# Kernel tuning notes

Hardware: AMD Instinct MI355X
Metric: run time of the kernel (lower is better)

## Reference

```python
import jax, jax.numpy as jnp
import numpy as np

HEADS = 4
C_HEAD = 32


def setup_inputs() -> dict:
    key = jax.random.key(0)
    k1, k2, k3 = jax.random.split(key, 3)
    c_in = 256
    c_hid = HEADS * C_HEAD  # 128
    x = jax.random.normal(k1, (4, c_in, 64, 64), dtype=jnp.float32)
    # 1x1 conv weights stored as [out, in]
    w_qkv = jax.random.normal(k2, (3 * c_hid, c_in), dtype=jnp.float32) * (c_in ** -0.5)
    w_out = jax.random.normal(k3, (c_in, c_hid), dtype=jnp.float32) * (c_hid ** -0.5)
    b_out = jnp.zeros((c_in,), dtype=jnp.float32)
    return {"x": x, "w_qkv": w_qkv, "w_out": w_out, "b_out": b_out}


def reference(x, w_qkv, w_out, b_out):
    b, c, h, w = x.shape
    scale = C_HEAD ** -0.5
    # 1x1 conv == channel matmul
    qkv = jnp.einsum('bchw,oc->bohw', x, w_qkv)  # [b, 3*c_hid, h, w]
    q, k, v = jnp.split(qkv, 3, axis=1)
    # b (heads c_head) x y -> b heads c_head (x y)
    def to_heads(t):
        return t.reshape(b, HEADS, C_HEAD, h * w)
    q, k, v = to_heads(q) * scale, to_heads(k), to_heads(v)
    sim = jnp.einsum('bhci,bhcj->bhij', q, k)  # [b, heads, N, N]
    sim = sim - jax.lax.stop_gradient(jnp.max(sim, axis=-1, keepdims=True))
    attn = jax.nn.softmax(sim, axis=-1)
    out = jnp.einsum('bhij,bhcj->bhic', attn, v)  # [b, heads, N, c_head]
    # b h (x y) c -> b (h c) x y
    out = out.transpose(0, 1, 3, 2).reshape(b, HEADS * C_HEAD, h, w)
    out = jnp.einsum('bchw,oc->bohw', out, w_out) + b_out[None, :, None, None]
    return out
```

## Files before the change

kernel.cpp:

```cpp
#include <hip/hip_runtime.h>
#include <hip/hip_bf16.h>
#include <cstdint>
#include <cstddef>


#define NB 4
#define CIN 256
#define CHID 128
#define HEADS 4
#define CHEAD 32
#define NPOS 4096
#define BH 16
#define NTOT 16384
#define QKV_O 384
#define QSCALE_LOG2E 0.2550348229f

typedef float f32x2 __attribute__((ext_vector_type(2)));
typedef float f32x4 __attribute__((ext_vector_type(4)));
typedef float f32x16 __attribute__((ext_vector_type(16)));
typedef short s16x8 __attribute__((ext_vector_type(8)));

static __device__ __forceinline__ unsigned short f2bf(float f) {
    union { float f; unsigned u; } v; v.f = f;
    unsigned r = v.u + 0x7FFFu + ((v.u >> 16) & 1u);
    return (unsigned short)(r >> 16);
}

static __device__ __forceinline__ unsigned int pk2bf(float a, float b) {
    union { __hip_bfloat162 h; unsigned int u; } c;
    c.h = __float22bfloat162_rn(float2{a, b});
    return c.u;
}

static __device__ __forceinline__ void plswap(unsigned& a, unsigned& b) {
#if __has_builtin(__builtin_amdgcn_permlane32_swap)
    auto r = __builtin_amdgcn_permlane32_swap((int)a, (int)b, false, false);
    a = (unsigned)r[0];
    b = (unsigned)r[1];
#else
    int hh = (threadIdx.x >> 5) & 1;
    unsigned ta = (unsigned)__shfl_xor((int)a, 32);
    unsigned tb = (unsigned)__shfl_xor((int)b, 32);
    unsigned na = hh ? tb : a;
    unsigned nb = hh ? b : ta;
    a = na; b = nb;
#endif
}

static __device__ __forceinline__ s16x8 mk8(unsigned a, unsigned b, unsigned c, unsigned d) {
    union { unsigned u[4]; s16x8 v; } x;
    x.u[0] = a; x.u[1] = b; x.u[2] = c; x.u[3] = d;
    return x.v;
}

static __device__ __forceinline__ void async_cp16(const void* g, void* l) {
    __builtin_amdgcn_global_load_lds((const __attribute__((address_space(1))) unsigned int*)g,
                                     (__attribute__((address_space(3))) unsigned int*)l, 16, 0, 0);
}

#define MFMA32(a, b, c) __builtin_amdgcn_mfma_f32_32x32x16_bf16(a, b, c, 0, 0, 0)


#define TBLOCKS (NB * (CIN / 32) * (NPOS / 32))
__global__ __launch_bounds__(256) void k_prep(const float* __restrict__ x,
                                              unsigned short* __restrict__ xT,
                                              const float* __restrict__ wqkv,
                                              const float* __restrict__ wout,
                                              unsigned short* __restrict__ wqkv_bf,
                                              unsigned short* __restrict__ wout_bf) {
    if (blockIdx.x >= TBLOCKS) {
        int i = (blockIdx.x - TBLOCKS) * 256 + threadIdx.x;
        if (i < QKV_O * CIN) wqkv_bf[i] = f2bf(wqkv[i]);
        if (i < CIN * CHID)  wout_bf[i] = f2bf(wout[i]);
        return;
    }
    __shared__ float tile[32][33];
    const int ntiles = NPOS / 32;
    const int ctiles = CIN / 32;
    int b   = blockIdx.x / (ntiles * ctiles);
    int rem = blockIdx.x % (ntiles * ctiles);
    int ct = rem / ntiles;
    int nt = rem % ntiles;
    int c0 = ct * 32, n0 = nt * 32;
    int tc = threadIdx.x / 32;
    int tn = threadIdx.x % 32;
    const float* xb = x + (size_t)b * CIN * NPOS;
#pragma unroll
    for (int it = 0; it < 4; ++it) {
        int c = tc + it * 8;
        tile[c][tn] = xb[(size_t)(c0 + c) * NPOS + n0 + tn];
    }
    __syncthreads();
    unsigned short* xTb = xT + (size_t)b * NPOS * CIN;
#pragma unroll
    for (int it = 0; it < 4; ++it) {
        int n = tc + it * 8;
        xTb[(size_t)(n0 + n) * CIN + c0 + tn] = f2bf(tile[tn][n]);
    }
}

__global__ __launch_bounds__(256, 4) void k_qkv(const unsigned short* __restrict__ wq,
                                                const unsigned short* __restrict__ xT,
                                                unsigned short* __restrict__ Q,
                                                unsigned short* __restrict__ K,
                                                unsigned short* __restrict__ V) {
    __shared__ __align__(16) unsigned char smem[2 * 12288];
    int mt = blockIdx.x % 3;
    int nt = blockIdx.x / 3;
    int wid = threadIdx.x >> 6, lane = threadIdx.x & 63;
    int quad = lane >> 4, low4 = lane & 15;
    int o0 = mt * 128, n0 = nt * 64;
    int lb = lane * 16;

    const unsigned short* srcA0 = wq + (size_t)(o0 + wid * 32 + low4) * CIN + quad * 8;
    const unsigned short* srcA1 = srcA0 + 16 * CIN;
    const unsigned short* srcB  = xT + (size_t)(n0 + wid * 16 + low4) * CIN + quad * 8;
    int dA0 = wid * 2048, dA1 = dA0 + 1024, dB = 8192 + wid * 1024;

    async_cp16(srcA0, smem + dA0 + lb);
    async_cp16(srcA1, smem + dA1 + lb);
    async_cp16(srcB,  smem + dB  + lb);
    __syncthreads();

    f32x4 acc[2][4] = {};
    for (int c = 0; c < 8; ++c) {
        if (c < 7) {
            unsigned char* nxt = smem + ((c + 1) & 1) * 12288;
            async_cp16(srcA0 + (c + 1) * 32, nxt + dA0 + lb);
            async_cp16(srcA1 + (c + 1) * 32, nxt + dA1 + lb);
            async_cp16(srcB  + (c + 1) * 32, nxt + dB  + lb);
        }
        const unsigned char* cur = smem + (c & 1) * 12288;
        s16x8 a0 = *(const s16x8*)(cur + wid * 2048 + lb);
        s16x8 a1 = *(const s16x8*)(cur + wid * 2048 + 1024 + lb);
#pragma unroll
        for (int j = 0; j < 4; ++j) {
            s16x8 bj = *(const s16x8*)(cur + 8192 + j * 1024 + lb);
            acc[0][j] = __builtin_amdgcn_mfma_f32_16x16x32_bf16(a0, bj, acc[0][j], 0, 0, 0);
            acc[1][j] = __builtin_amdgcn_mfma_f32_16x16x32_bf16(a1, bj, acc[1][j], 0, 0, 0);
        }
        __syncthreads();
    }

    if (mt == 0) {
#pragma unroll
        for (int i = 0; i < 2; ++i) {
            int ol = wid * 32 + i * 16 + quad * 4;
            int head = ol >> 5, ch = ol & 31;
#pragma unroll
            for (int j = 0; j < 4; ++j) {
                int nG = n0 + j * 16 + low4;
                int b = nG >> 12, n = nG & 4095;
                f32x4 v = acc[i][j];
                unsigned long long d =
                    (unsigned long long)pk2bf(v[0] * QSCALE_LOG2E, v[1] * QSCALE_LOG2E) |
                    ((unsigned long long)pk2bf(v[2] * QSCALE_LOG2E, v[3] * QSCALE_LOG2E) << 32);
                *(unsigned long long*)(Q + ((size_t)(b * 4 + head) * NPOS + n) * 32 + ch) = d;
            }
        }
    } else if (mt == 1) {
#pragma unroll
        for (int i = 0; i < 2; ++i) {
            int ol = wid * 32 + i * 16 + quad * 4;
            int head = ol >> 5, c0 = ol & 31;
            int f = c0 >> 4, hh = (c0 >> 3) & 1, j8 = c0 & 7;
#pragma unroll
            for (int j = 0; j < 4; ++j) {
                int nG = n0 + j * 16 + low4;
                int b = nG >> 12, n = nG & 4095;
                int bh = b * 4 + head;
                f32x4 v = acc[i][j];
                unsigned long long d =
                    (unsigned long long)pk2bf(v[0], v[1]) |
                    ((unsigned long long)pk2bf(v[2], v[3]) << 32);
                size_t addr = (((size_t)bh * 128 + (n >> 5)) * 2 + f) * 512
                            + (size_t)((((hh << 5) | (n & 31)) << 3) + j8);
                *(unsigned long long*)(K + addr) = d;
            }
        }
    } else {
        unsigned short* vt = (unsigned short*)smem;
#pragma unroll
        for (int i = 0; i < 2; ++i) {
            int ol = wid * 32 + i * 16 + quad * 4;
#pragma unroll
            for (int j = 0; j < 4; ++j) {
                int col = j * 16 + low4;
#pragma unroll
                for (int r = 0; r < 4; ++r) vt[(ol + r) * 80 + col] = f2bf(acc[i][j][r]);
            }
        }
        __syncthreads();
        int b = n0 >> 12, nbase = n0 & 4095;
#pragma unroll
        for (int rep = 0; rep < 4; ++rep) {
            int idx = rep * 256 + threadIdx.x;
            int row = idx >> 3, c8 = idx & 7;
            s16x8 val = *(const s16x8*)(vt + row * 80 + c8 * 8);
            int head = row >> 5, ch = row & 31;
            int bh = b * 4 + head;
            int nstart = nbase + c8 * 8;
            int kc = nstart >> 4, hh = (nstart >> 3) & 1;
            *(s16x8*)(V + ((size_t)(bh * 256 + kc) * 64 + ((hh << 5) | ch)) * 8) = val;
        }
    }
}

__global__ __launch_bounds__(256, 4) void k_attn(const unsigned short* __restrict__ Q,
                                                 const unsigned short* __restrict__ K,
                                                 const unsigned short* __restrict__ V,
                                                 unsigned short* __restrict__ attnO) {
    __shared__ __align__(16) unsigned char smem[2 * 16384];
    int bh = blockIdx.x & 15;
    int qt = blockIdx.x >> 4;
    int wid = threadIdx.x >> 6;
    int lane = threadIdx.x & 63;
    int q5 = lane & 31, h = lane >> 5;
    int qg = wid & 1, kh = wid >> 1;
    int q0 = qt * 64 + qg * 32;
    int khk = kh * 2048;

    const unsigned short* Qp = Q + (size_t)bh * NPOS * 32;

    s16x8 bq0 = *(const s16x8*)(Qp + (size_t)(q0 + q5) * 32 + h * 8);
    s16x8 bq1 = *(const s16x8*)(Qp + (size_t)(q0 + q5) * 32 + 16 + h * 8);

    const unsigned short* pKf = K + (size_t)bh * 131072 + lane * 8;
    const unsigned short* pVf = V + (size_t)bh * 131072 + lane * 8;

    auto stage = [&](int bufi, int k0) {
        unsigned char* wb = smem + bufi * 16384 + kh * 8192;
        if (qg == 0) {
            const unsigned short* p = pKf + (size_t)(k0 >> 5) * 1024;
            async_cp16(p,        wb);
            async_cp16(p + 512,  wb + 1024);
            async_cp16(p + 1024, wb + 2048);
            async_cp16(p + 1536, wb + 3072);
        } else {
            const unsigned short* p = pVf + (size_t)(k0 >> 4) * 512;
            async_cp16(p,        wb + 4096);
            async_cp16(p + 512,  wb + 5120);
            async_cp16(p + 1024, wb + 6144);
            async_cp16(p + 1536, wb + 7168);
        }
    };

    f32x16 oT = {};
    f32x2 lacc0 = {0.0f, 0.0f}, lacc1 = {0.0f, 0.0f};
    const int lby = lane * 16;

    stage(0, khk);

#pragma unroll 1
    for (int it = 0; it < 32; ++it) {
        if (it + 1 < 32) {
            stage((it + 1) & 1, khk + (it + 1) * 64);
            asm volatile("s_waitcnt vmcnt(4)" ::: "memory");
        } else {
            asm volatile("s_waitcnt vmcnt(0)" ::: "memory");
        }
        asm volatile("s_barrier" ::: "memory");

        const unsigned char* kb = smem + (it & 1) * 16384 + kh * 8192;
#pragma unroll
        for (int t = 0; t < 2; ++t) {
            s16x8 ak0 = *(const s16x8*)(kb + t * 2048 + lby);
            s16x8 ak1 = *(const s16x8*)(kb + t * 2048 + 1024 + lby);
            f32x16 s = {};
            __builtin_amdgcn_s_setprio(1);
            s = MFMA32(ak0, bq0, s);
            s = MFMA32(ak1, bq1, s);
            __builtin_amdgcn_s_setprio(0);
            unsigned p[8];
#pragma unroll
            for (int i = 0; i < 8; ++i) {
                float e0 = __builtin_amdgcn_exp2f(s[2 * i]);
                float e1 = __builtin_amdgcn_exp2f(s[2 * i + 1]);
                f32x2 e = {e0, e1};
                if (i & 1) lacc0 += e;
                else       lacc1 += e;
                p[i] = pk2bf(e0, e1);
            }
            plswap(p[0], p[2]); plswap(p[1], p[3]);
            plswap(p[4], p[6]); plswap(p[5], p[7]);
            s16x8 bplo = mk8(p[0], p[1], p[2], p[3]);
            s16x8 bphi = mk8(p[4], p[5], p[6], p[7]);

            s16x8 av0 = *(const s16x8*)(kb + 4096 + (2 * t) * 1024 + lby);
            s16x8 av1 = *(const s16x8*)(kb + 4096 + (2 * t + 1) * 1024 + lby);
            __builtin_amdgcn_s_setprio(1);
            oT = MFMA32(av0, bplo, oT);
            oT = MFMA32(av1, bphi, oT);
            __builtin_amdgcn_s_setprio(0);
        }
        asm volatile("s_barrier" ::: "memory");
    }

    float lsum = lacc0[0] + lacc0[1] + lacc1[0] + lacc1[1];
    lsum += __shfl_xor(lsum, 32);

    if (kh) {
        float* area = (float*)(smem + qg * 4352);
#pragma unroll
        for (int j = 0; j < 4; ++j)
            *(f32x4*)(area + j * 256 + lane * 4) =
                f32x4{oT[4 * j], oT[4 * j + 1], oT[4 * j + 2], oT[4 * j + 3]};
        area[1024 + lane] = lsum;
    }
    __syncthreads();
    if (!kh) {
        const float* area = (const float*)(smem + qg * 4352);
        lsum += area[1024 + lane];
        float inv = 1.0f / lsum;
        int b = bh >> 2, head = bh & 3;
        int n = q0 + q5;
        unsigned short* base = attnO + ((size_t)(b * NPOS + n)) * CHID + head * 32 + 4 * h;
#pragma unroll
        for (int j = 0; j < 4; ++j) {
            f32x4 r = *(const f32x4*)(area + j * 256 + lane * 4);
            unsigned long long d =
                (unsigned long long)pk2bf((oT[4 * j] + r[0]) * inv, (oT[4 * j + 1] + r[1]) * inv) |
                ((unsigned long long)pk2bf((oT[4 * j + 2] + r[2]) * inv, (oT[4 * j + 3] + r[3]) * inv) << 32);
            *(unsigned long long*)(base + 8 * j) = d;
        }
    }
}

__global__ __launch_bounds__(256, 4) void k_out(const unsigned short* __restrict__ wo,
                                                const unsigned short* __restrict__ attnO,
                                                const float* __restrict__ bias,
                                                float* __restrict__ out) {
    __shared__ __align__(16) unsigned char smem[2 * 12288];
    int mt = blockIdx.x & 1;
    int nt = blockIdx.x >> 1;
    int wid = threadIdx.x >> 6, lane = threadIdx.x & 63;
    int quad = lane >> 4, low4 = lane & 15;
    int o0 = mt * 128, n0 = nt * 64;
    int lb = lane * 16;

    const unsigned short* srcA0 = wo + (size_t)(o0 + wid * 32 + low4) * CHID + quad * 8;
    const unsigned short* srcA1 = srcA0 + 16 * CHID;
    const unsigned short* srcB  = attnO + (size_t)(n0 + wid * 16 + low4) * CHID + quad * 8;
    int dA0 = wid * 2048, dA1 = dA0 + 1024, dB = 8192 + wid * 1024;

    async_cp16(srcA0, smem + dA0 + lb);
    async_cp16(srcA1, smem + dA1 + lb);
    async_cp16(srcB,  smem + dB  + lb);
    __syncthreads();

    f32x4 acc[2][4] = {};
    for (int c = 0; c < 4; ++c) {
        if (c < 3) {
            unsigned char* nxt = smem + ((c + 1) & 1) * 12288;
            async_cp16(srcA0 + (c + 1) * 32, nxt + dA0 + lb);
            async_cp16(srcA1 + (c + 1) * 32, nxt + dA1 + lb);
            async_cp16(srcB  + (c + 1) * 32, nxt + dB  + lb);
        }
        const unsigned char* cur = smem + (c & 1) * 12288;
        s16x8 a0 = *(const s16x8*)(cur + wid * 2048 + lb);
        s16x8 a1 = *(const s16x8*)(cur + wid * 2048 + 1024 + lb);
#pragma unroll
        for (int j = 0; j < 4; ++j) {
            s16x8 bj = *(const s16x8*)(cur + 8192 + j * 1024 + lb);
            acc[0][j] = __builtin_amdgcn_mfma_f32_16x16x32_bf16(a0, bj, acc[0][j], 0, 0, 0);
            acc[1][j] = __builtin_amdgcn_mfma_f32_16x16x32_bf16(a1, bj, acc[1][j], 0, 0, 0);
        }
        __syncthreads();
    }

#pragma unroll
    for (int i = 0; i < 2; ++i) {
        int ob = o0 + wid * 32 + i * 16 + quad * 4;
#pragma unroll
        for (int j = 0; j < 4; ++j) {
            int nG = n0 + j * 16 + low4;
            int b = nG >> 12, n = nG & 4095;
#pragma unroll
            for (int r = 0; r < 4; ++r) {
                int o = ob + r;
                out[((size_t)(b * CIN + o)) * NPOS + n] = acc[i][j][r] + bias[o];
            }
        }
    }
}

extern "C" void kernel_launch(void* const* d_in, const int* in_sizes, int n_in,
                              void* d_out, int out_size, void* d_ws, size_t ws_size,
                              hipStream_t stream) {
    const float* x    = (const float*)d_in[0];
    const float* wqkv = (const float*)d_in[1];
    const float* wout = (const float*)d_in[2];
    const float* bout = (const float*)d_in[3];
    float* out = (float*)d_out;

    unsigned short* Q       = (unsigned short*)d_ws;
    unsigned short* K       = Q + (size_t)BH * NPOS * 32;
    unsigned short* V       = K + (size_t)BH * NPOS * 32;
    unsigned short* attnO   = V + (size_t)BH * 32 * NPOS;
    unsigned short* xT      = attnO + (size_t)NTOT * CHID;
    unsigned short* wqkv_bf = xT + (size_t)NTOT * CIN;
    unsigned short* wout_bf = wqkv_bf + QKV_O * CIN;

    k_prep<<<TBLOCKS + (QKV_O * CIN + 255) / 256, 256, 0, stream>>>(x, xT, wqkv, wout, wqkv_bf, wout_bf);
    k_qkv<<<3 * (NTOT / 64), 256, 0, stream>>>(wqkv_bf, xT, Q, K, V);
    k_attn<<<(NPOS / 64) * BH, 256, 0, stream>>>(Q, K, V, attnO);
    k_out<<<2 * (NTOT / 64), 256, 0, stream>>>(wout_bf, attnO, bout, out);
}
```

Measured before the change: 155.7 us.

## Stage epilogues through LDS for wide coalesced stores in prep, qkv, out

The x transpose kernel moves to 64x64 tiles with float4 loads and 16-byte packed bf16 stores. The Q and K epilogues in the qkv kernel now transpose through shared memory so each thread writes 16-byte chunks instead of scattered 8-byte writes. The output projection epilogue stages fp32 results in LDS, in two halves, so it can emit float4 row-contiguous stores instead of strided scalar stores. The aim is to cut uncoalesced global write traffic in the memory-bound stages, at the price of extra LDS round trips and barriers.

After: 157.0 us. About the same (+0.8%).

```diff
diff --git a/kernel.cpp b/kernel.cpp
--- a/kernel.cpp
+++ b/kernel.cpp
@@ -61,41 +61,47 @@
 #define MFMA32(a, b, c) __builtin_amdgcn_mfma_f32_32x32x16_bf16(a, b, c, 0, 0, 0)
 
 
-#define TBLOCKS (NB * (CIN / 32) * (NPOS / 32))
+#define PTILES (NB * (CIN / 64) * (NPOS / 64))
 __global__ __launch_bounds__(256) void k_prep(const float* __restrict__ x,
                                               unsigned short* __restrict__ xT,
                                               const float* __restrict__ wqkv,
                                               const float* __restrict__ wout,
                                               unsigned short* __restrict__ wqkv_bf,
                                               unsigned short* __restrict__ wout_bf) {
-    if (blockIdx.x >= TBLOCKS) {
-        int i = (blockIdx.x - TBLOCKS) * 256 + threadIdx.x;
+    if (blockIdx.x >= PTILES) {
+        int i = (blockIdx.x - PTILES) * 256 + threadIdx.x;
         if (i < QKV_O * CIN) wqkv_bf[i] = f2bf(wqkv[i]);
         if (i < CIN * CHID)  wout_bf[i] = f2bf(wout[i]);
         return;
     }
-    __shared__ float tile[32][33];
-    const int ntiles = NPOS / 32;
-    const int ctiles = CIN / 32;
-    int b   = blockIdx.x / (ntiles * ctiles);
-    int rem = blockIdx.x % (ntiles * ctiles);
-    int ct = rem / ntiles;
-    int nt = rem % ntiles;
-    int c0 = ct * 32, n0 = nt * 32;
-    int tc = threadIdx.x / 32;
-    int tn = threadIdx.x % 32;
+    __shared__ float tile[64][65];
+    const int per_b = (CIN / 64) * (NPOS / 64);
+    int b   = blockIdx.x / per_b;
+    int rem = blockIdx.x % per_b;
+    int ct = rem / (NPOS / 64);
+    int nt = rem % (NPOS / 64);
+    int c0 = ct * 64, n0 = nt * 64;
+    int t = threadIdx.x;
     const float* xb = x + (size_t)b * CIN * NPOS;
 #pragma unroll
     for (int it = 0; it < 4; ++it) {
-        int c = tc + it * 8;
-        tile[c][tn] = xb[(size_t)(c0 + c) * NPOS + n0 + tn];
+        int c  = (t >> 4) + it * 16;
+        int n4 = (t & 15) * 4;
+        f32x4 v = *(const f32x4*)(xb + (size_t)(c0 + c) * NPOS + n0 + n4);
+        tile[c][n4] = v[0]; tile[c][n4 + 1] = v[1];
+        tile[c][n4 + 2] = v[2]; tile[c][n4 + 3] = v[3];
     }
     __syncthreads();
     unsigned short* xTb = xT + (size_t)b * NPOS * CIN;
 #pragma unroll
-    for (int it = 0; it < 4; ++it) {
-        int n = tc + it * 8;
-        xTb[(size_t)(n0 + n) * CIN + c0 + tn] = f2bf(tile[tn][n]);
+    for (int it = 0; it < 2; ++it) {
+        int slot = it * 256 + t;
+        int n  = slot >> 3;
+        int c8 = (slot & 7) * 8;
+        union { unsigned short u[8]; s16x8 v; } pk;
+#pragma unroll
+        for (int r = 0; r < 8; ++r) pk.u[r] = f2bf(tile[c8 + r][n]);
+        *(s16x8*)(xTb + (size_t)(n0 + n) * CIN + c0 + c8) = pk.v;
     }
 }
 
@@ -142,47 +148,53 @@
         __syncthreads();
     }
 
-    if (mt == 0) {
+    int b = n0 >> 12, nbase = n0 & 4095;
+    if (mt < 2) {
+        unsigned short (*vtT)[136] = (unsigned short(*)[136])smem;
+        float sc = (mt == 0) ? QSCALE_LOG2E : 1.0f;
+#pragma unroll
+        for (int i = 0; i < 2; ++i) {
+            int ob = wid * 32 + i * 16 + quad * 4;
+#pragma unroll
+            for (int j = 0; j < 4; ++j) {
+                int nl = j * 16 + low4;
+                f32x4 v = acc[i][j];
+                unsigned long long d =
+                    (unsigned long long)pk2bf(v[0] * sc, v[1] * sc) |
+                    ((unsigned long long)pk2bf(v[2] * sc, v[3] * sc) << 32);
+                *(unsigned long long*)(&vtT[nl][ob]) = d;
+            }
+        }
+        __syncthreads();
+        if (mt == 0) {
+#pragma unroll
+            for (int it = 0; it < 4; ++it) {
+                int slot = it * 256 + threadIdx.x;
+                int n = slot >> 4, c16 = slot & 15;
+                s16x8 val = *(const s16x8*)(&vtT[n][c16 * 8]);
+                int o = c16 * 8, head = o >> 5, ch = o & 31;
+                *(s16x8*)(Q + ((size_t)(b * 4 + head) * NPOS + nbase + n) * 32 + ch) = val;
+            }
+        } else {
+#pragma unroll
+            for (int it = 0; it < 4; ++it) {
+                int slot = it * 256 + threadIdx.x;
+                int c16 = slot >> 6, n = slot & 63;
+                s16x8 val = *(const s16x8*)(&vtT[n][c16 * 8]);
+                int o = c16 * 8, head = o >> 5, c0h = o & 31;
+                int f = c0h >> 4, hh = (c0h >> 3) & 1;
+                int nG = nbase + n;
+                int bh = b * 4 + head;
+                size_t addr = (((size_t)bh * 128 + (nG >> 5)) * 2 + f) * 512
+                            + (size_t)((((hh << 5) | (nG & 31)) << 3));
+                *(s16x8*)(K + addr) = val;
+            }
+        }
+    } else {
+        unsigned short* vt = (unsigned short*)smem;
 #pragma unroll
         for (int i = 0; i < 2; ++i) {
             int ol = wid * 32 + i * 16 + quad * 4;
-            int head = ol >> 5, ch = ol & 31;
-#pragma unroll
-            for (int j = 0; j < 4; ++j) {
-                int nG = n0 + j * 16 + low4;
-                int b = nG >> 12, n = nG & 4095;
-                f32x4 v = acc[i][j];
-                unsigned long long d =
-                    (unsigned long long)pk2bf(v[0] * QSCALE_LOG2E, v[1] * QSCALE_LOG2E) |
-                    ((unsigned long long)pk2bf(v[2] * QSCALE_LOG2E, v[3] * QSCALE_LOG2E) << 32);
-                *(unsigned long long*)(Q + ((size_t)(b * 4 + head) * NPOS + n) * 32 + ch) = d;
-            }
-        }
-    } else if (mt == 1) {
-#pragma unroll
-        for (int i = 0; i < 2; ++i) {
-            int ol = wid * 32 + i * 16 + quad * 4;
-            int head = ol >> 5, c0 = ol & 31;
-            int f = c0 >> 4, hh = (c0 >> 3) & 1, j8 = c0 & 7;
-#pragma unroll
-            for (int j = 0; j < 4; ++j) {
-                int nG = n0 + j * 16 + low4;
-                int b = nG >> 12, n = nG & 4095;
-                int bh = b * 4 + head;
-                f32x4 v = acc[i][j];
-                unsigned long long d =
-                    (unsigned long long)pk2bf(v[0], v[1]) |
-                    ((unsigned long long)pk2bf(v[2], v[3]) << 32);
-                size_t addr = (((size_t)bh * 128 + (n >> 5)) * 2 + f) * 512
-                            + (size_t)((((hh << 5) | (n & 31)) << 3) + j8);
-                *(unsigned long long*)(K + addr) = d;
-            }
-        }
-    } else {
-        unsigned short* vt = (unsigned short*)smem;
-#pragma unroll
-        for (int i = 0; i < 2; ++i) {
-            int ol = wid * 32 + i * 16 + quad * 4;
 #pragma unroll
             for (int j = 0; j < 4; ++j) {
                 int col = j * 16 + low4;
@@ -191,7 +203,6 @@
             }
         }
         __syncthreads();
-        int b = n0 >> 12, nbase = n0 & 4095;
 #pragma unroll
         for (int rep = 0; rep < 4; ++rep) {
             int idx = rep * 256 + threadIdx.x;
@@ -368,19 +379,34 @@
         __syncthreads();
     }
 
-#pragma unroll
-    for (int i = 0; i < 2; ++i) {
-        int ob = o0 + wid * 32 + i * 16 + quad * 4;
-#pragma unroll
-        for (int j = 0; j < 4; ++j) {
-            int nG = n0 + j * 16 + low4;
-            int b = nG >> 12, n = nG & 4095;
-#pragma unroll
-            for (int r = 0; r < 4; ++r) {
-                int o = ob + r;
-                out[((size_t)(b * CIN + o)) * NPOS + n] = acc[i][j][r] + bias[o];
-            }
-        }
+    float (*larea)[68] = (float(*)[68])smem;
+    int b = n0 >> 12, nb = n0 & 4095;
+#pragma unroll
+    for (int half = 0; half < 2; ++half) {
+        if ((wid >> 1) == half) {
+#pragma unroll
+            for (int i = 0; i < 2; ++i) {
+                int row = (wid & 1) * 32 + i * 16 + quad * 4;
+                int o = o0 + half * 64 + row;
+#pragma unroll
+                for (int j = 0; j < 4; ++j) {
+                    int nl = j * 16 + low4;
+#pragma unroll
+                    for (int r = 0; r < 4; ++r)
+                        larea[row + r][nl] = acc[i][j][r] + bias[o + r];
+                }
+            }
+        }
+        __syncthreads();
+#pragma unroll
+        for (int it = 0; it < 4; ++it) {
+            int slot = it * 256 + threadIdx.x;
+            int row = slot >> 4, nn4 = (slot & 15) * 4;
+            int o = o0 + half * 64 + row;
+            f32x4 v = *(const f32x4*)(&larea[row][nn4]);
+            *(f32x4*)(out + ((size_t)(b * CIN + o)) * NPOS + nb + nn4) = v;
+        }
+        __syncthreads();
     }
 }
 
@@ -401,7 +427,7 @@
     unsigned short* wqkv_bf = xT + (size_t)NTOT * CIN;
     unsigned short* wout_bf = wqkv_bf + QKV_O * CIN;
 
-    k_prep<<<TBLOCKS + (QKV_O * CIN + 255) / 256, 256, 0, stream>>>(x, xT, wqkv, wout, wqkv_bf, wout_bf);
+    k_prep<<<PTILES + (QKV_O * CIN + 255) / 256, 256, 0, stream>>>(x, xT, wqkv, wout, wqkv_bf, wout_bf);
     k_qkv<<<3 * (NTOT / 64), 256, 0, stream>>>(wqkv_bf, xT, Q, K, V);
     k_attn<<<(NPOS / 64) * BH, 256, 0, stream>>>(Q, K, V, attnO);
     k_out<<<2 * (NTOT / 64), 256, 0, stream>>>(wout_bf, attnO, bout, out);
```
